# Kernel tuning notes

Hardware: AMD Instinct MI355X
Metric: run time of the kernel (lower is better)

## Reference

```python
import jax, jax.numpy as jnp
import numpy as np


def setup_inputs() -> dict:
    key = jax.random.key(0)
    k1, k2, k3, k4 = jax.random.split(key, 4)
    TOKENS, D_IN, D_OUT = 8192, 4096, 4096
    x = jax.random.normal(k1, (TOKENS, D_IN), dtype=jnp.float32)
    # stored quantized weight: integer-valued codes held in a float buffer
    weight = jax.random.randint(k2, (D_OUT, D_IN), 0, 127).astype(jnp.float32)
    bias = jax.random.normal(k3, (D_OUT,), dtype=jnp.float32)
    weight_scale = jax.random.uniform(k4, (), dtype=jnp.float32)
    return {"x": x, "weight": weight, "bias": bias, "weight_scale": weight_scale}


def reference(x, weight, bias, weight_scale):
    # Dequantize: W_fp = W * scale, then y = x @ W_fp^T + b
    # (original casts to double only for dtype compatibility; same math)
    weight_fp = weight * weight_scale  # [out, in]
    return jnp.einsum("ti,oi->to", x, weight_fp) + bias
```

## Files before the change

### kernel.cpp

```cpp
#include <hip/hip_runtime.h>
#include <hip/hip_bf16.h>


typedef __bf16 bf16_t;
typedef __attribute__((ext_vector_type(8))) __bf16 bf16x8;
typedef __attribute__((ext_vector_type(4))) __bf16 bf16x4;
typedef __attribute__((ext_vector_type(4))) float f32x4;

#define BM 128
#define BN 128
#define BK 32

#define LDS_U32(p) ((__attribute__((address_space(3))) uint32_t*)(p))
#define GLB_U32(p) ((const __attribute__((address_space(1))) uint32_t*)(p))
#define ASM_BARRIER() asm volatile("s_barrier" ::: "memory")
#define LGKM0() asm volatile("s_waitcnt lgkmcnt(0)" ::: "memory")

__global__ __launch_bounds__(256)
void cvt2_f32_bf16(const float* __restrict__ xsrc, bf16_t* __restrict__ xdst, long xn8,
                   const float* __restrict__ wsrc, bf16_t* __restrict__ wdst, long wn8)
{
    long i = (long)blockIdx.x * 256 + threadIdx.x;
    const float4* s;
    bf16x8* d;
    if (i < xn8) {
        s = (const float4*)xsrc; d = (bf16x8*)xdst;
    } else {
        i -= xn8;
        if (i >= wn8) return;
        s = (const float4*)wsrc; d = (bf16x8*)wdst;
    }
    float4 a = s[2 * i];
    float4 b = s[2 * i + 1];
    bf16x8 o = { (bf16_t)a.x, (bf16_t)a.y, (bf16_t)a.z, (bf16_t)a.w,
                 (bf16_t)b.x, (bf16_t)b.y, (bf16_t)b.z, (bf16_t)b.w };
    d[i] = o;
}

__global__ __launch_bounds__(512, 2)
void ql_gemm_256_8ph(const bf16_t* __restrict__ X,
                     const bf16_t* __restrict__ W,
                     const float* __restrict__ bias,
                     const float* __restrict__ scale_p,
                     float* __restrict__ Y,
                     int M, int N, int K)
{
    __shared__ alignas(16) bf16_t lds[2][2][2][256][32];
    static_assert(sizeof(lds) == 131072, "LDS layout");

    const int tid    = threadIdx.x;
    const int lane   = tid & 63;
    const int wid    = tid >> 6;
    const int wr     = wid >> 2;
    const int wc     = wid & 3;
    const int r_lane = lane & 15;
    const int quad   = lane >> 4;
    const int rd_col = (quad ^ ((r_lane >> 1) & 3)) * 8;

    const int st_row = lane >> 2;
    const int st_col = ((lane & 3) ^ ((lane >> 3) & 3)) * 8;

    const int rbA1 = (wid & 3) * 16 + wr * 128;
    const int rbA2 = rbA1 + 64;
    const int rbB1 = (wid & 1) * 16 + (wid >> 1) * 64;
    const int rbB2 = rbB1 + 32;

    int bid = blockIdx.x;
    const int nbn = N >> 8;
    const int nwg = gridDim.x;
    if ((nwg & 7) == 0) { const int q = nwg >> 3; bid = (bid & 7) * q + (bid >> 3); }
    const int m0 = (bid / nbn) << 8;
    const int n0 = (bid % nbn) << 8;

    const int NT = K >> 6;

    const bf16_t* pA1 = X + (size_t)(m0 + rbA1 + st_row) * K + st_col;
    const bf16_t* pA2 = X + (size_t)(m0 + rbA2 + st_row) * K + st_col;
    const bf16_t* pB1 = W + (size_t)(n0 + rbB1 + st_row) * K + st_col;
    const bf16_t* pB2 = W + (size_t)(n0 + rbB2 + st_row) * K + st_col;

#define STG(PTR, BUFC, MATC, RB)                                              \
    do {                                                                      \
        __builtin_amdgcn_global_load_lds(GLB_U32(PTR),                        \
            LDS_U32(&lds[BUFC][MATC][0][RB][0]), 16, 0, 0);                   \
        __builtin_amdgcn_global_load_lds(GLB_U32((PTR) + 32),                 \
            LDS_U32(&lds[BUFC][MATC][1][RB][0]), 16, 0, 0);                   \
    } while (0)

    f32x4 acc[8][4];
#pragma unroll
    for (int i = 0; i < 8; i++)
#pragma unroll
        for (int j = 0; j < 4; j++)
            acc[i][j] = (f32x4)0.0f;

    STG(pA1, 0, 0, rbA1);
    STG(pB1, 0, 1, rbB1);
    STG(pB2, 0, 1, rbB2);
    STG(pA2, 0, 0, rbA2);
    STG(pA1 + 64, 1, 0, rbA1);
    STG(pB1 + 64, 1, 1, rbB1);
    STG(pB2 + 64, 1, 1, rbB2);
    pA2 += 64;
    pA1 += 128;
    pB1 += 128;
    pB2 += 128;
    asm volatile("s_waitcnt vmcnt(6)" ::: "memory");
    ASM_BARRIER();

    bf16x8 aA[4][2], aB0[2][2], aB1[2][2];

#define KTILE(BUFC, DOA2, DOREST, WN)                                         \
    do {                                                                      \
                            \
        if (DOA2) { STG(pA2, (BUFC) ^ 1, 0, rbA2); pA2 += 64; }               \
        _Pragma("unroll") for (int i = 0; i < 4; i++)                         \
        _Pragma("unroll") for (int kk = 0; kk < 2; kk++)                      \
            aA[i][kk] = *(const bf16x8*)&lds[BUFC][0][kk][wr * 128 + i * 16 + r_lane][rd_col]; \
        _Pragma("unroll") for (int j = 0; j < 2; j++)                         \
        _Pragma("unroll") for (int kk = 0; kk < 2; kk++)                      \
            aB0[j][kk] = *(const bf16x8*)&lds[BUFC][1][kk][wc * 64 + j * 16 + r_lane][rd_col]; \
        LGKM0();                                                              \
        ASM_BARRIER();                                                        \
        __builtin_amdgcn_s_setprio(1);                                        \
        _Pragma("unroll") for (int i = 0; i < 4; i++)                         \
        _Pragma("unroll") for (int j = 0; j < 2; j++)                         \
        _Pragma("unroll") for (int kk = 0; kk < 2; kk++)                      \
            acc[i][j] = __builtin_amdgcn_mfma_f32_16x16x32_bf16(              \
                aA[i][kk], aB0[j][kk], acc[i][j], 0, 0, 0);                   \
        __builtin_amdgcn_s_setprio(0);                                        \
                    \
        if (DOREST) { STG(pA1, BUFC, 0, rbA1); pA1 += 64; }                   \
        _Pragma("unroll") for (int j = 0; j < 2; j++)                         \
        _Pragma("unroll") for (int kk = 0; kk < 2; kk++)                      \
            aB1[j][kk] = *(const bf16x8*)&lds[BUFC][1][kk][wc * 64 + (2 + j) * 16 + r_lane][rd_col]; \
        LGKM0();                                                              \
        ASM_BARRIER();                                                        \
        __builtin_amdgcn_s_setprio(1);                                        \
        _Pragma("unroll") for (int i = 0; i < 4; i++)                         \
        _Pragma("unroll") for (int j = 0; j < 2; j++)                         \
        _Pragma("unroll") for (int kk = 0; kk < 2; kk++)                      \
            acc[i][2 + j] = __builtin_amdgcn_mfma_f32_16x16x32_bf16(          \
                aA[i][kk], aB1[j][kk], acc[i][2 + j], 0, 0, 0);               \
        __builtin_amdgcn_s_setprio(0);                                        \
                  \
        if (DOREST) { STG(pB1, BUFC, 1, rbB1); pB1 += 64; }                   \
        _Pragma("unroll") for (int i = 0; i < 4; i++)                         \
        _Pragma("unroll") for (int kk = 0; kk < 2; kk++)                      \
            aA[i][kk] = *(const bf16x8*)&lds[BUFC][0][kk][wr * 128 + (4 + i) * 16 + r_lane][rd_col]; \
        LGKM0();                                                              \
        ASM_BARRIER();                                                        \
        __builtin_amdgcn_s_setprio(1);                                        \
        _Pragma("unroll") for (int i = 0; i < 4; i++)                         \
        _Pragma("unroll") for (int j = 0; j < 2; j++)                         \
        _Pragma("unroll") for (int kk = 0; kk < 2; kk++)                      \
            acc[4 + i][j] = __builtin_amdgcn_mfma_f32_16x16x32_bf16(          \
                aA[i][kk], aB0[j][kk], acc[4 + i][j], 0, 0, 0);               \
        __builtin_amdgcn_s_setprio(0);                                        \
                  \
        if (DOREST) { STG(pB2, BUFC, 1, rbB2); pB2 += 64; }                   \
         \
         \
                                                 \
        asm volatile("s_waitcnt vmcnt(%0)" :: "n"(WN) : "memory");            \
        ASM_BARRIER();                                                        \
        __builtin_amdgcn_s_setprio(1);                                        \
        _Pragma("unroll") for (int i = 0; i < 4; i++)                         \
        _Pragma("unroll") for (int j = 0; j < 2; j++)                         \
        _Pragma("unroll") for (int kk = 0; kk < 2; kk++)                      \
            acc[4 + i][2 + j] = __builtin_amdgcn_mfma_f32_16x16x32_bf16(      \
                aA[i][kk], aB1[j][kk], acc[4 + i][2 + j], 0, 0, 0);           \
        __builtin_amdgcn_s_setprio(0);                                        \
    } while (0)

    for (int t = 0; t + 3 < NT; t += 2) {
        KTILE(0, 1, 1, 6);
        KTILE(1, 1, 1, 6);
    }
    KTILE(0, 1, 0, 0);
    KTILE(1, 0, 0, 0);
#undef KTILE
#undef STG

    const float s = *scale_p;
#pragma unroll
    for (int j = 0; j < 4; j++) {
        const int col  = n0 + wc * 64 + j * 16 + r_lane;
        const float bc = bias[col];
#pragma unroll
        for (int i = 0; i < 8; i++) {
            const int rowg = m0 + wr * 128 + i * 16 + quad * 4;
#pragma unroll
            for (int r = 0; r < 4; r++)
                Y[(size_t)(rowg + r) * N + col] = acc[i][j][r] * s + bc;
        }
    }
}

__global__ __launch_bounds__(256)
void ql_gemm_bf16_dma(const bf16_t* __restrict__ X,
                      const bf16_t* __restrict__ W,
                      const float* __restrict__ bias,
                      const float* __restrict__ scale_p,
                      float* __restrict__ Y,
                      int M, int N, int K)
{
    __shared__ alignas(16) bf16_t lA[BM][BK];
    __shared__ alignas(16) bf16_t lB[BN][BK];

    const int tid  = threadIdx.x;
    const int lane = tid & 63;
    const int wave = tid >> 6;
    const int wm   = (wave & 1) * 64;
    const int wn   = (wave >> 1) * 64;

    const int m0 = blockIdx.x * BM;
    const int n0 = blockIdx.y * BN;

    const int r_lane = lane & 15;
    const int quad   = lane >> 4;

    const int st_row = lane >> 2;
    const int st_q   = (lane & 3) ^ ((lane >> 3) & 3);
    const int st_col = st_q * 8;

    const int rd_col = (quad ^ ((r_lane >> 1) & 3)) * 8;

    f32x4 acc[4][4];
#pragma unroll
    for (int i = 0; i < 4; i++)
#pragma unroll
        for (int j = 0; j < 4; j++)
            acc[i][j] = (f32x4)0.0f;

    for (int k0 = 0; k0 < K; k0 += BK) {
#pragma unroll
        for (int i = 0; i < 2; i++) {
            const int c   = i * 4 + wave;
            const int row = c * 16 + st_row;
            __builtin_amdgcn_global_load_lds(
                GLB_U32(X + (size_t)(m0 + row) * K + k0 + st_col),
                LDS_U32(&lA[c * 16][0]), 16, 0, 0);
            __builtin_amdgcn_global_load_lds(
                GLB_U32(W + (size_t)(n0 + row) * K + k0 + st_col),
                LDS_U32(&lB[c * 16][0]), 16, 0, 0);
        }
        __syncthreads();

        bf16x8 af[4], bfr[4];
#pragma unroll
        for (int i = 0; i < 4; i++) {
            af[i]  = *(const bf16x8*)&lA[wm + i * 16 + r_lane][rd_col];
            bfr[i] = *(const bf16x8*)&lB[wn + i * 16 + r_lane][rd_col];
        }

#pragma unroll
        for (int i = 0; i < 4; i++)
#pragma unroll
            for (int j = 0; j < 4; j++)
                acc[i][j] = __builtin_amdgcn_mfma_f32_16x16x32_bf16(
                    af[i], bfr[j], acc[i][j], 0, 0, 0);

        __syncthreads();
    }

    const float s = *scale_p;
#pragma unroll
    for (int j = 0; j < 4; j++) {
        const int col  = n0 + wn + j * 16 + r_lane;
        const float bc = bias[col];
#pragma unroll
        for (int i = 0; i < 4; i++) {
            const int rowg = m0 + wm + i * 16 + quad * 4;
#pragma unroll
            for (int r = 0; r < 4; r++)
                Y[(size_t)(rowg + r) * N + col] = acc[i][j][r] * s + bc;
        }
    }
}

__global__ __launch_bounds__(256)
void ql_gemm_bf16_fused(const float* __restrict__ X, const float* __restrict__ W,
                        const float* __restrict__ bias, const float* __restrict__ scale_p,
                        float* __restrict__ Y, int M, int N, int K)
{
    __shared__ alignas(16) bf16_t lA[BM][BK];
    __shared__ alignas(16) bf16_t lB[BN][BK];

    const int tid  = threadIdx.x;
    const int lane = tid & 63;
    const int wave = tid >> 6;
    const int wm   = (wave & 1) * 64;
    const int wn   = (wave >> 1) * 64;
    const int m0 = blockIdx.x * BM;
    const int n0 = blockIdx.y * BN;
    const int r_lane = lane & 15;
    const int quad   = lane >> 4;

    f32x4 acc[4][4];
#pragma unroll
    for (int i = 0; i < 4; i++)
#pragma unroll
        for (int j = 0; j < 4; j++) acc[i][j] = (f32x4)0.0f;

    for (int k0 = 0; k0 < K; k0 += BK) {
#pragma unroll
        for (int i = 0; i < 4; i++) {
            const int l   = tid + i * 256;
            const int row = l >> 3;
            const int c4  = (l & 7) * 4;
            const float4 xa = *(const float4*)(X + (size_t)(m0 + row) * K + k0 + c4);
            const float4 wb = *(const float4*)(W + (size_t)(n0 + row) * K + k0 + c4);
            bf16x4 xh = { (bf16_t)xa.x, (bf16_t)xa.y, (bf16_t)xa.z, (bf16_t)xa.w };
            bf16x4 wh = { (bf16_t)wb.x, (bf16_t)wb.y, (bf16_t)wb.z, (bf16_t)wb.w };
            *(bf16x4*)&lA[row][c4] = xh;
            *(bf16x4*)&lB[row][c4] = wh;
        }
        __syncthreads();
        bf16x8 af[4], bfr[4];
#pragma unroll
        for (int i = 0; i < 4; i++) {
            af[i]  = *(const bf16x8*)&lA[wm + i * 16 + r_lane][quad * 8];
            bfr[i] = *(const bf16x8*)&lB[wn + i * 16 + r_lane][quad * 8];
        }
#pragma unroll
        for (int i = 0; i < 4; i++)
#pragma unroll
            for (int j = 0; j < 4; j++)
                acc[i][j] = __builtin_amdgcn_mfma_f32_16x16x32_bf16(af[i], bfr[j], acc[i][j], 0, 0, 0);
        __syncthreads();
    }

    const float s = *scale_p;
#pragma unroll
    for (int j = 0; j < 4; j++) {
        const int col  = n0 + wn + j * 16 + r_lane;
        const float bc = bias[col];
#pragma unroll
        for (int i = 0; i < 4; i++) {
            const int rowg = m0 + wm + i * 16 + quad * 4;
#pragma unroll
            for (int r = 0; r < 4; r++)
                Y[(size_t)(rowg + r) * N + col] = acc[i][j][r] * s + bc;
        }
    }
}

extern "C" void kernel_launch(void* const* d_in, const int* in_sizes, int n_in,
                              void* d_out, int out_size, void* d_ws, size_t ws_size,
                              hipStream_t stream) {
    const float* X     = (const float*)d_in[0];
    const float* W     = (const float*)d_in[1];
    const float* bias  = (const float*)d_in[2];
    const float* scale = (const float*)d_in[3];
    float* Y           = (float*)d_out;

    const int N = in_sizes[2];
    const int K = in_sizes[1] / N;
    const int M = in_sizes[0] / K;

    const size_t x_elems = (size_t)M * K;
    const size_t w_elems = (size_t)N * K;
    const size_t need = (x_elems + w_elems) * sizeof(bf16_t);

    if (ws_size >= need) {
        bf16_t* Xb = (bf16_t*)d_ws;
        bf16_t* Wb = Xb + x_elems;
        long xn8 = (long)(x_elems / 8);
        long wn8 = (long)(w_elems / 8);
        long nthreads = xn8 + wn8;
        cvt2_f32_bf16<<<(nthreads + 255) / 256, 256, 0, stream>>>(X, Xb, xn8, W, Wb, wn8);

        if ((M % 256 == 0) && (N % 256 == 0) && (K % 128 == 0) && (K >= 256) &&
            (x_elems % 8 == 0) && (w_elems % 8 == 0)) {
            dim3 grid((M / 256) * (N / 256));
            ql_gemm_256_8ph<<<grid, 512, 0, stream>>>(Xb, Wb, bias, scale, Y, M, N, K);
        } else {
            dim3 grid(M / BM, N / BN);
            ql_gemm_bf16_dma<<<grid, 256, 0, stream>>>(Xb, Wb, bias, scale, Y, M, N, K);
        }
    } else {
        dim3 grid(M / BM, N / BN);
        ql_gemm_bf16_fused<<<grid, 256, 0, stream>>>(X, W, bias, scale, Y, M, N, K);
    }
}
```

Before: 489.2 us.

## Prefetch next k-tile LDS fragments across stages with partial lgkmcnt waits

Restructures the GEMM main loop so LDS fragment reads for the next k-tile (A low half, B first half) are issued during the current tile's later MFMA phases. A second register set for the upper A rows is added, and waits become partial lgkmcnt/vmcnt counts instead of full drains. This is meant to hide LDS read latency behind MFMA work. It costs extra VGPRs and makes the barrier and wait-count logic more fragile.

```diff
diff --git a/kernel.cpp b/kernel.cpp
--- a/kernel.cpp
+++ b/kernel.cpp
@@ -14,7 +14,6 @@
 #define LDS_U32(p) ((__attribute__((address_space(3))) uint32_t*)(p))
 #define GLB_U32(p) ((const __attribute__((address_space(1))) uint32_t*)(p))
 #define ASM_BARRIER() asm volatile("s_barrier" ::: "memory")
-#define LGKM0() asm volatile("s_waitcnt lgkmcnt(0)" ::: "memory")
 
 __global__ __launch_bounds__(256)
 void cvt2_f32_bf16(const float* __restrict__ xsrc, bf16_t* __restrict__ xdst, long xn8,
@@ -105,22 +104,32 @@
     pA1 += 128;
     pB1 += 128;
     pB2 += 128;
-    asm volatile("s_waitcnt vmcnt(6)" ::: "memory");
+    asm volatile("s_waitcnt vmcnt(8)" ::: "memory");
     ASM_BARRIER();
 
-    bf16x8 aA[4][2], aB0[2][2], aB1[2][2];
-
-#define KTILE(BUFC, DOA2, DOREST, WN)                                         \
+    bf16x8 aA[4][2], aAhi[4][2], aB0[2][2], aB1[2][2];
+
+#pragma unroll
+    for (int i = 0; i < 4; i++)
+#pragma unroll
+        for (int kk = 0; kk < 2; kk++)
+            aA[i][kk] = *(const bf16x8*)&lds[0][0][kk][wr * 128 + i * 16 + r_lane][rd_col];
+#pragma unroll
+    for (int j = 0; j < 2; j++)
+#pragma unroll
+        for (int kk = 0; kk < 2; kk++)
+            aB0[j][kk] = *(const bf16x8*)&lds[0][1][kk][wc * 64 + j * 16 + r_lane][rd_col];
+
+#define KTILE(BUFC, DOA2, DOREST, DONEXT, WTOP, WMID)                         \
     do {                                                                      \
-                            \
+                                     \
         if (DOA2) { STG(pA2, (BUFC) ^ 1, 0, rbA2); pA2 += 64; }               \
-        _Pragma("unroll") for (int i = 0; i < 4; i++)                         \
-        _Pragma("unroll") for (int kk = 0; kk < 2; kk++)                      \
-            aA[i][kk] = *(const bf16x8*)&lds[BUFC][0][kk][wr * 128 + i * 16 + r_lane][rd_col]; \
+                                        \
         _Pragma("unroll") for (int j = 0; j < 2; j++)                         \
         _Pragma("unroll") for (int kk = 0; kk < 2; kk++)                      \
-            aB0[j][kk] = *(const bf16x8*)&lds[BUFC][1][kk][wc * 64 + j * 16 + r_lane][rd_col]; \
-        LGKM0();                                                              \
+            aB1[j][kk] = *(const bf16x8*)&lds[BUFC][1][kk][wc * 64 + (2 + j) * 16 + r_lane][rd_col]; \
+                \
+        asm volatile("s_waitcnt lgkmcnt(4) vmcnt(%0)" :: "n"(WTOP) : "memory"); \
         ASM_BARRIER();                                                        \
         __builtin_amdgcn_s_setprio(1);                                        \
         _Pragma("unroll") for (int i = 0; i < 4; i++)                         \
@@ -129,12 +138,14 @@
             acc[i][j] = __builtin_amdgcn_mfma_f32_16x16x32_bf16(              \
                 aA[i][kk], aB0[j][kk], acc[i][j], 0, 0, 0);                   \
         __builtin_amdgcn_s_setprio(0);                                        \
-                    \
+                        \
         if (DOREST) { STG(pA1, BUFC, 0, rbA1); pA1 += 64; }                   \
-        _Pragma("unroll") for (int j = 0; j < 2; j++)                         \
-        _Pragma("unroll") for (int kk = 0; kk < 2; kk++)                      \
-            aB1[j][kk] = *(const bf16x8*)&lds[BUFC][1][kk][wc * 64 + (2 + j) * 16 + r_lane][rd_col]; \
-        LGKM0();                                                              \
+                                      \
+        _Pragma("unroll") for (int i = 0; i < 4; i++)                         \
+        _Pragma("unroll") for (int kk = 0; kk < 2; kk++)                      \
+            aAhi[i][kk] = *(const bf16x8*)&lds[BUFC][0][kk][wr * 128 + (4 + i) * 16 + r_lane][rd_col]; \
+                                  \
+        asm volatile("s_waitcnt lgkmcnt(8)" ::: "memory");                    \
         ASM_BARRIER();                                                        \
         __builtin_amdgcn_s_setprio(1);                                        \
         _Pragma("unroll") for (int i = 0; i < 4; i++)                         \
@@ -143,42 +154,49 @@
             acc[i][2 + j] = __builtin_amdgcn_mfma_f32_16x16x32_bf16(          \
                 aA[i][kk], aB1[j][kk], acc[i][2 + j], 0, 0, 0);               \
         __builtin_amdgcn_s_setprio(0);                                        \
-                  \
+                       \
         if (DOREST) { STG(pB1, BUFC, 1, rbB1); pB1 += 64; }                   \
-        _Pragma("unroll") for (int i = 0; i < 4; i++)                         \
-        _Pragma("unroll") for (int kk = 0; kk < 2; kk++)                      \
-            aA[i][kk] = *(const bf16x8*)&lds[BUFC][0][kk][wr * 128 + (4 + i) * 16 + r_lane][rd_col]; \
-        LGKM0();                                                              \
+        \
+                              \
+        asm volatile("s_waitcnt lgkmcnt(0) vmcnt(%0)" :: "n"(WMID) : "memory"); \
         ASM_BARRIER();                                                        \
+         \
+        if (DONEXT) {                                                         \
+            _Pragma("unroll") for (int i = 0; i < 4; i++)                     \
+            _Pragma("unroll") for (int kk = 0; kk < 2; kk++)                  \
+                aA[i][kk] = *(const bf16x8*)&lds[(BUFC) ^ 1][0][kk][wr * 128 + i * 16 + r_lane][rd_col]; \
+        }                                                                     \
         __builtin_amdgcn_s_setprio(1);                                        \
         _Pragma("unroll") for (int i = 0; i < 4; i++)                         \
         _Pragma("unroll") for (int j = 0; j < 2; j++)                         \
         _Pragma("unroll") for (int kk = 0; kk < 2; kk++)                      \
             acc[4 + i][j] = __builtin_amdgcn_mfma_f32_16x16x32_bf16(          \
-                aA[i][kk], aB0[j][kk], acc[4 + i][j], 0, 0, 0);               \
+                aAhi[i][kk], aB0[j][kk], acc[4 + i][j], 0, 0, 0);             \
         __builtin_amdgcn_s_setprio(0);                                        \
-                  \
+                \
         if (DOREST) { STG(pB2, BUFC, 1, rbB2); pB2 += 64; }                   \
+        ASM_BARRIER();                                                        \
          \
-         \
-                                                 \
-        asm volatile("s_waitcnt vmcnt(%0)" :: "n"(WN) : "memory");            \
-        ASM_BARRIER();                                                        \
+        if (DONEXT) {                                                         \
+            _Pragma("unroll") for (int j = 0; j < 2; j++)                     \
+            _Pragma("unroll") for (int kk = 0; kk < 2; kk++)                  \
+                aB0[j][kk] = *(const bf16x8*)&lds[(BUFC) ^ 1][1][kk][wc * 64 + j * 16 + r_lane][rd_col]; \
+        }                                                                     \
         __builtin_amdgcn_s_setprio(1);                                        \
         _Pragma("unroll") for (int i = 0; i < 4; i++)                         \
         _Pragma("unroll") for (int j = 0; j < 2; j++)                         \
         _Pragma("unroll") for (int kk = 0; kk < 2; kk++)                      \
             acc[4 + i][2 + j] = __builtin_amdgcn_mfma_f32_16x16x32_bf16(      \
-                aA[i][kk], aB1[j][kk], acc[4 + i][2 + j], 0, 0, 0);           \
+                aAhi[i][kk], aB1[j][kk], acc[4 + i][2 + j], 0, 0, 0);         \
         __builtin_amdgcn_s_setprio(0);                                        \
     } while (0)
 
     for (int t = 0; t + 3 < NT; t += 2) {
-        KTILE(0, 1, 1, 6);
-        KTILE(1, 1, 1, 6);
-    }
-    KTILE(0, 1, 0, 0);
-    KTILE(1, 0, 0, 0);
+        KTILE(0, 1, 1, 1, 8, 6);
+        KTILE(1, 1, 1, 1, 8, 6);
+    }
+    KTILE(0, 1, 0, 1, 8, 2);
+    KTILE(1, 0, 0, 0, 0, 0);
 #undef KTILE
 #undef STG
 
```

Result: slower. 692.4 us (+41.5%).
